# Kernel tuning notes

Hardware: AMD Instinct MI355X
Metric: run time of the kernel (lower is better)

## Reference

```python
import jax, jax.numpy as jnp
import numpy as np
import math

D = 1024
H = 16
EPS = 1e-5

def _layernorm(x, gamma, beta):
    mu = jnp.mean(x, axis=-1, keepdims=True)
    var = jnp.var(x, axis=-1, keepdims=True)
    return (x - mu) * jax.lax.rsqrt(var + EPS) * gamma + beta

def setup_inputs() -> dict:
    key = jax.random.key(0)
    ks = jax.random.split(key, 6)
    B, T = 2, 2048
    x = jax.random.normal(ks[0], (B, T, D), dtype=jnp.float32)
    s = 1.0 / math.sqrt(D)
    Wq = jax.random.normal(ks[1], (D, D), dtype=jnp.float32) * s
    Wk = jax.random.normal(ks[2], (D, D), dtype=jnp.float32) * s
    Wv = jax.random.normal(ks[3], (D, D), dtype=jnp.float32) * s
    gamma = jnp.ones((D,), dtype=jnp.float32)
    beta = jnp.zeros((D,), dtype=jnp.float32)
    return {"x": x, "Wq": Wq, "Wk": Wk, "Wv": Wv, "gamma": gamma, "beta": beta}

def reference(x, Wq, Wk, Wv, gamma, beta):
    B, T, Dm = x.shape
    hd = Dm // H
    xn = _layernorm(x, gamma, beta)
    # torch Linear (no bias): y = x @ W.T
    q = (xn @ Wq.T).reshape(B, T, H, hd)
    k = (xn @ Wk.T).reshape(B, T, H, hd)
    v = (xn @ Wv.T).reshape(B, T, H, hd)
    scale = 1.0 / math.sqrt(hd)
    att = jnp.einsum('bnhd,bmhd->bnmh', q, k) * scale  # B,T,T,H
    w = jax.nn.softmax(att, axis=2)  # softmax over key dim m
    y = jnp.einsum('bnmh,bmhd->bnhd', w, v).reshape(B, T, Dm)
    return x + y
```

## Files before the change

### kernel.cpp

```cpp
#include <hip/hip_runtime.h>
#include <hip/hip_bf16.h>
#include <stdint.h>

#define D_MODEL 1024
#define T_SEQ   2048
#define NB      2
#define NH      16
#define HD      64
#define MTOK    4096

typedef __bf16  bf16x8 __attribute__((ext_vector_type(8)));
typedef float   f32x4  __attribute__((ext_vector_type(4)));
typedef float   f32x16 __attribute__((ext_vector_type(16)));

#define GPTR(p) ((const __attribute__((address_space(1))) void*)(p))
#define LPTR(p) ((__attribute__((address_space(3))) void*)(p))

static __device__ __forceinline__ ushort f2bf(float f) {
    union { float f; uint32_t u; } c{f};
    uint32_t u = c.u;
    return (ushort)((u + 0x7fff + ((u >> 16) & 1)) >> 16);
}

static __device__ __forceinline__ unsigned cvt_pk_bf16(float lo, float hi) {
    unsigned r;
    asm("v_cvt_pk_bf16_f32 %0, %1, %2" : "=v"(r) : "v"(lo), "v"(hi));
    return r;
}

#if defined(__has_builtin)
#if __has_builtin(__builtin_amdgcn_exp2f)
#define FEXP2(x) __builtin_amdgcn_exp2f(x)
#endif
#endif
#ifndef FEXP2
static __device__ __forceinline__ float fexp2_asm(float x) {
    float r;
    asm("v_exp_f32 %0, %1" : "=v"(r) : "v"(x));
    return r;
}
#define FEXP2(x) fexp2_asm(x)
#endif

__global__ __launch_bounds__(256) void ln_kernel(const float* __restrict__ x,
                                                 const float* __restrict__ gamma,
                                                 const float* __restrict__ beta,
                                                 ushort* __restrict__ xn) {
    int row = blockIdx.x;
    int tid = threadIdx.x;
    const float4* xr = (const float4*)(x + (size_t)row * D_MODEL);
    float4 v = xr[tid];
    float s  = v.x + v.y + v.z + v.w;
    float ss = v.x * v.x + v.y * v.y + v.z * v.z + v.w * v.w;
    #pragma unroll
    for (int m = 1; m < 64; m <<= 1) {
        s  += __shfl_xor(s, m);
        ss += __shfl_xor(ss, m);
    }
    __shared__ float red[8];
    int w = tid >> 6, lane = tid & 63;
    if (lane == 0) { red[w] = s; red[4 + w] = ss; }
    __syncthreads();
    s  = red[0] + red[1] + red[2] + red[3];
    ss = red[4] + red[5] + red[6] + red[7];
    float mu   = s * (1.0f / D_MODEL);
    float var  = ss * (1.0f / D_MODEL) - mu * mu;
    float rstd = rsqrtf(var + 1e-5f);
    float4 g = ((const float4*)gamma)[tid];
    float4 b = ((const float4*)beta)[tid];
    ushort4 o;
    o.x = f2bf((v.x - mu) * rstd * g.x + b.x);
    o.y = f2bf((v.y - mu) * rstd * g.y + b.y);
    o.z = f2bf((v.z - mu) * rstd * g.z + b.z);
    o.w = f2bf((v.w - mu) * rstd * g.w + b.w);
    ((ushort4*)(xn + (size_t)row * D_MODEL))[tid] = o;
}

__global__ __launch_bounds__(256) void cvt3_kernel(const float* __restrict__ a0,
                                                   const float* __restrict__ a1,
                                                   const float* __restrict__ a2,
                                                   ushort* __restrict__ o0,
                                                   ushort* __restrict__ o1,
                                                   ushort* __restrict__ o2) {
    int z = blockIdx.y;
    const float* a = (z == 0) ? a0 : (z == 1) ? a1 : a2;
    ushort* o = (z == 0) ? o0 : (z == 1) ? o1 : o2;
    int i = blockIdx.x * 256 + threadIdx.x;
    float4 v = ((const float4*)a)[i];
    ushort4 r;
    r.x = f2bf(v.x); r.y = f2bf(v.y); r.z = f2bf(v.z); r.w = f2bf(v.w);
    ((ushort4*)o)[i] = r;
}

__global__ __launch_bounds__(256) void gemm_qkv(const ushort* __restrict__ A,
                                                const ushort* __restrict__ w0,
                                                const ushort* __restrict__ w1,
                                                const ushort* __restrict__ w2,
                                                ushort* __restrict__ c0,
                                                ushort* __restrict__ c1,
                                                ushort* __restrict__ c2,
                                                int M, int N, int K) {
    const ushort* Bw = (blockIdx.z == 0) ? w0 : (blockIdx.z == 1) ? w1 : w2;
    ushort* C = (blockIdx.z == 0) ? c0 : (blockIdx.z == 1) ? c1 : c2;

    __shared__ __align__(16) ushort lA[128 * 64];
    __shared__ __align__(16) ushort lB[128 * 64];
    int tid = threadIdx.x;
    int w = tid >> 6, lane = tid & 63;
    int wr = w >> 1, wc = w & 1;
    int l15 = lane & 15, l4 = lane >> 4;
    int row0 = blockIdx.x * 128, col0 = blockIdx.y * 128;

    f32x4 zero = {0.f, 0.f, 0.f, 0.f};
    f32x4 acc[4][4];
    #pragma unroll
    for (int i = 0; i < 4; ++i)
        #pragma unroll
        for (int j = 0; j < 4; ++j) acc[i][j] = zero;

    int s_row = (tid * 16) >> 7;
    int s_col = ((tid * 16) & 127) >> 1;

    for (int kt = 0; kt < K / 64; ++kt) {
        int k0 = kt * 64;
        __syncthreads();
        #pragma unroll
        for (int i = 0; i < 4; ++i) {
            int r = s_row + i * 32;
            const ushort* ga = A + (size_t)(row0 + r) * K + k0 + s_col;
            __builtin_amdgcn_global_load_lds(GPTR(ga), LPTR((char*)lA + i * 4096 + w * 1024), 16, 0, 0);
            const ushort* gb = Bw + (size_t)(col0 + r) * K + k0 + s_col;
            __builtin_amdgcn_global_load_lds(GPTR(gb), LPTR((char*)lB + i * 4096 + w * 1024), 16, 0, 0);
        }
        __syncthreads();
        #pragma unroll
        for (int ks = 0; ks < 2; ++ks) {
            bf16x8 af[4], bfr[4];
            #pragma unroll
            for (int i = 0; i < 4; ++i) {
                af[i]  = *(const bf16x8*)&lA[(wr * 64 + i * 16 + l15) * 64 + ks * 32 + l4 * 8];
                bfr[i] = *(const bf16x8*)&lB[(wc * 64 + i * 16 + l15) * 64 + ks * 32 + l4 * 8];
            }
            #pragma unroll
            for (int i = 0; i < 4; ++i)
                #pragma unroll
                for (int j = 0; j < 4; ++j)
                    acc[i][j] = __builtin_amdgcn_mfma_f32_16x16x32_bf16(af[i], bfr[j], acc[i][j], 0, 0, 0);
        }
    }
    if (blockIdx.z == 2) {
        #pragma unroll
        for (int i = 0; i < 4; ++i) {
            int rbase = row0 + wr * 64 + i * 16 + l4 * 4;
            #pragma unroll
            for (int j = 0; j < 4; ++j) {
                int col = col0 + wc * 64 + j * 16 + l15;
                ushort4 o4;
                o4.x = f2bf(acc[i][j][0]);
                o4.y = f2bf(acc[i][j][1]);
                o4.z = f2bf(acc[i][j][2]);
                o4.w = f2bf(acc[i][j][3]);
                *(ushort4*)&C[(size_t)col * M + rbase] = o4;
            }
        }
    } else {
        float sc = (blockIdx.z == 0) ? 0.18033688011112042f : 1.0f;
        #pragma unroll
        for (int i = 0; i < 4; ++i) {
            int rbase = row0 + wr * 64 + i * 16 + l4 * 4;
            #pragma unroll
            for (int j = 0; j < 4; ++j) {
                int col = col0 + wc * 64 + j * 16 + l15;
                #pragma unroll
                for (int r = 0; r < 4; ++r)
                    C[(size_t)(rbase + r) * N + col] = f2bf(acc[i][j][r] * sc);
            }
        }
    }
}

__global__ __launch_bounds__(256, 2) void attn_kernel(const ushort* __restrict__ Q,
                                                      const ushort* __restrict__ Km,
                                                      const ushort* __restrict__ Vt,
                                                      const float* __restrict__ x,
                                                      float* __restrict__ out) {
    int bid = blockIdx.x;
    int sw  = (bid & 7) * 64 + (bid >> 3);
    int qt = sw & 15, h = (sw >> 4) & 15, b = sw >> 8;

    int tid = threadIdx.x, w = tid >> 6, lane = tid & 63;
    int l31 = lane & 31, hh = lane >> 5, x7 = lane & 7;
    size_t head_off = (size_t)b * T_SEQ * D_MODEL + (size_t)h * HD;
    const ushort* Qh  = Q  + head_off;
    const ushort* Kh  = Km + head_off;
    const ushort* Vth = Vt + (size_t)h * HD * MTOK + (size_t)b * T_SEQ;

    __shared__ __align__(16) ushort lK[4][64 * 64];
    __shared__ __align__(16) ushort lV[4][64 * 64];

    int qrow = qt * 128 + w * 32 + l31;
    bf16x8 qf[4];
    #pragma unroll
    for (int c = 0; c < 4; ++c)
        qf[c] = *(const bf16x8*)&Qh[(size_t)qrow * D_MODEL + hh * 8 + c * 16];

    int i0  = w * 128 + lane;
    int r0  = i0 >> 3;
    int cg0 = (i0 & 7) ^ (r0 & 7);
    const ushort* ksrc0 = Kh  + (size_t)r0 * D_MODEL + cg0 * 8;
    const ushort* ksrc1 = ksrc0 + (size_t)8 * D_MODEL;
    const ushort* vsrc0 = Vth + (size_t)r0 * MTOK + cg0 * 8;
    const ushort* vsrc1 = vsrc0 + (size_t)8 * MTOK;

    int chv[4];
    #pragma unroll
    for (int c = 0; c < 4; ++c) chv[c] = ((hh + 2 * c) ^ x7) << 4;

    f32x16 oa[2], ob[2], zvec;
    float la = 0.f, lb = 0.f;
    #pragma unroll
    for (int i = 0; i < 16; ++i) {
        oa[0][i] = 0.f; oa[1][i] = 0.f; ob[0][i] = 0.f; ob[1][i] = 0.f;
        zvec[i] = 0.f;
    }

    auto STAGE = [&](int t) {
        size_t kb = (size_t)t * 64;
        char* dk = (char*)lK[t & 3] + w * 2048;
        char* dv = (char*)lV[t & 3] + w * 2048;
        __builtin_amdgcn_global_load_lds(GPTR(ksrc0 + kb * D_MODEL), LPTR(dk), 16, 0, 0);
        __builtin_amdgcn_global_load_lds(GPTR(ksrc1 + kb * D_MODEL), LPTR(dk + 1024), 16, 0, 0);
        __builtin_amdgcn_global_load_lds(GPTR(vsrc0 + kb), LPTR(dv), 16, 0, 0);
        __builtin_amdgcn_global_load_lds(GPTR(vsrc1 + kb), LPTR(dv + 1024), 16, 0, 0);
    };

    auto QK = [&](int t, f32x16& sa, f32x16& sb) {
        const char* lKc = (const char*)lK[t & 3];
        __builtin_amdgcn_s_setprio(1);
        {
            bf16x8 ka  = *(const bf16x8*)(lKc + l31 * 128 + chv[0]);
            bf16x8 kb2 = *(const bf16x8*)(lKc + (32 + l31) * 128 + chv[0]);
            sa = __builtin_amdgcn_mfma_f32_32x32x16_bf16(ka,  qf[0], zvec, 0, 0, 0);
            sb = __builtin_amdgcn_mfma_f32_32x32x16_bf16(kb2, qf[0], zvec, 0, 0, 0);
        }
        #pragma unroll
        for (int c = 1; c < 4; ++c) {
            bf16x8 ka  = *(const bf16x8*)(lKc + l31 * 128 + chv[c]);
            bf16x8 kb2 = *(const bf16x8*)(lKc + (32 + l31) * 128 + chv[c]);
            sa = __builtin_amdgcn_mfma_f32_32x32x16_bf16(ka,  qf[c], sa, 0, 0, 0);
            sb = __builtin_amdgcn_mfma_f32_32x32x16_bf16(kb2, qf[c], sb, 0, 0, 0);
        }
        __builtin_amdgcn_s_setprio(0);
    };

    auto SMPV = [&](int t, const f32x16& sa, const f32x16& sb) {
        const char* lVc = (const char*)lV[t & 3];
        bf16x8 pfr[4];
        #pragma unroll
        for (int kbb = 0; kbb < 2; ++kbb) {
            float pr[16];
            #pragma unroll
            for (int r = 0; r < 16; ++r) pr[r] = FEXP2(kbb ? sb[r] : sa[r]);
            float s0 = (pr[0] + pr[1]) + (pr[2] + pr[3]);
            float s1 = (pr[4] + pr[5]) + (pr[6] + pr[7]);
            float s2 = (pr[8] + pr[9]) + (pr[10] + pr[11]);
            float s3 = (pr[12] + pr[13]) + (pr[14] + pr[15]);
            if (kbb == 0) la += (s0 + s1) + (s2 + s3);
            else          lb += (s0 + s1) + (s2 + s3);
            #pragma unroll
            for (int sl = 0; sl < 2; ++sl) {
                unsigned pA = cvt_pk_bf16(pr[sl * 8 + 0], pr[sl * 8 + 1]);
                unsigned pB = cvt_pk_bf16(pr[sl * 8 + 2], pr[sl * 8 + 3]);
                unsigned pC = cvt_pk_bf16(pr[sl * 8 + 4], pr[sl * 8 + 5]);
                unsigned pD = cvt_pk_bf16(pr[sl * 8 + 6], pr[sl * 8 + 7]);
                asm("v_permlane32_swap_b32 %0, %1" : "+v"(pA), "+v"(pC));
                asm("v_permlane32_swap_b32 %0, %1" : "+v"(pB), "+v"(pD));
                union { unsigned u[4]; bf16x8 v; } pf;
                pf.u[0] = pA; pf.u[1] = pB; pf.u[2] = pC; pf.u[3] = pD;
                pfr[kbb * 2 + sl] = pf.v;
            }
        }
        __builtin_amdgcn_s_setprio(1);
        #pragma unroll
        for (int ks = 0; ks < 4; ++ks) {
            #pragma unroll
            for (int dblk = 0; dblk < 2; ++dblk) {
                bf16x8 vf = *(const bf16x8*)(lVc + (dblk * 32 + l31) * 128 + chv[ks]);
                if (ks & 1)
                    ob[dblk] = __builtin_amdgcn_mfma_f32_32x32x16_bf16(vf, pfr[ks], ob[dblk], 0, 0, 0);
                else
                    oa[dblk] = __builtin_amdgcn_mfma_f32_32x32x16_bf16(vf, pfr[ks], oa[dblk], 0, 0, 0);
            }
        }
        __builtin_amdgcn_s_setprio(0);
    };

    STAGE(0);
    STAGE(1);
    __syncthreads();

    const int NT = T_SEQ / 64;
    for (int s = 0; s < NT / 2; ++s) {
        int t0 = 2 * s;
        if (s < NT / 2 - 1) { STAGE(t0 + 2); STAGE(t0 + 3); }
        f32x16 sa0, sb0, sa1, sb1;
        QK(t0, sa0, sb0);
        QK(t0 + 1, sa1, sb1);
        SMPV(t0, sa0, sb0);
        SMPV(t0 + 1, sa1, sb1);
        __syncthreads();
    }

    float Lt = la + lb;
    float Lfull = Lt + __shfl_xor(Lt, 32);
    float inv = 1.0f / Lfull;
    const float* xrow = x   + (size_t)(b * T_SEQ + qrow) * D_MODEL + h * HD + 4 * hh;
    float*       orow = out + (size_t)(b * T_SEQ + qrow) * D_MODEL + h * HD + 4 * hh;
    #pragma unroll
    for (int dblk = 0; dblk < 2; ++dblk) {
        #pragma unroll
        for (int g = 0; g < 4; ++g) {
            int coff = dblk * 32 + 8 * g;
            float4 xv = *(const float4*)(xrow + coff);
            float4 ov;
            ov.x = xv.x + (oa[dblk][4 * g + 0] + ob[dblk][4 * g + 0]) * inv;
            ov.y = xv.y + (oa[dblk][4 * g + 1] + ob[dblk][4 * g + 1]) * inv;
            ov.z = xv.z + (oa[dblk][4 * g + 2] + ob[dblk][4 * g + 2]) * inv;
            ov.w = xv.w + (oa[dblk][4 * g + 3] + ob[dblk][4 * g + 3]) * inv;
            *(float4*)(orow + coff) = ov;
        }
    }
}

extern "C" void kernel_launch(void* const* d_in, const int* in_sizes, int n_in,
                              void* d_out, int out_size, void* d_ws, size_t ws_size,
                              hipStream_t stream) {
    const float* x     = (const float*)d_in[0];
    const float* Wq    = (const float*)d_in[1];
    const float* Wk    = (const float*)d_in[2];
    const float* Wv    = (const float*)d_in[3];
    const float* gamma = (const float*)d_in[4];
    const float* beta  = (const float*)d_in[5];
    float* out = (float*)d_out;

    char* ws = (char*)d_ws;
    ushort* xn  = (ushort*)(ws);
    ushort* wqb = (ushort*)(ws + (8  << 20));
    ushort* wkb = (ushort*)(ws + (10 << 20));
    ushort* wvb = (ushort*)(ws + (12 << 20));
    ushort* Qb  = (ushort*)(ws + (14 << 20));
    ushort* Kb  = (ushort*)(ws + (22 << 20));
    ushort* Vtb = (ushort*)(ws + (30 << 20));

    int M = NB * T_SEQ;

    cvt3_kernel<<<dim3(1024, 3), 256, 0, stream>>>(Wq, Wk, Wv, wqb, wkb, wvb);
    ln_kernel<<<dim3(M), 256, 0, stream>>>(x, gamma, beta, xn);
    gemm_qkv<<<dim3(M / 128, D_MODEL / 128, 3), 256, 0, stream>>>(
        xn, wqb, wkb, wvb, Qb, Kb, Vtb, M, D_MODEL, D_MODEL);
    attn_kernel<<<dim3(512), 256, 0, stream>>>(Qb, Kb, Vtb, x, out);
}
```

Baseline: 110.0 us.

## Double-buffer QKV GEMM LDS tiles with XOR swizzle and MFMA priority

The QKV projection GEMM now stages its tiles through double-buffered LDS, prefetching the next K tile while the current one is consumed. This removes one barrier per iteration and overlaps global-to-LDS loads with MFMA work. The LDS layout is XOR-swizzled by row to avoid bank conflicts on fragment reads, and s_setprio raises wave priority around the MFMA section. LDS use doubles to 64KB per block, which may reduce occupancy.

```diff
diff --git a/kernel.cpp b/kernel.cpp
--- a/kernel.cpp
+++ b/kernel.cpp
@@ -103,8 +103,8 @@
     const ushort* Bw = (blockIdx.z == 0) ? w0 : (blockIdx.z == 1) ? w1 : w2;
     ushort* C = (blockIdx.z == 0) ? c0 : (blockIdx.z == 1) ? c1 : c2;
 
-    __shared__ __align__(16) ushort lA[128 * 64];
-    __shared__ __align__(16) ushort lB[128 * 64];
+    __shared__ __align__(16) ushort lA[2][128 * 64];
+    __shared__ __align__(16) ushort lB[2][128 * 64];
     int tid = threadIdx.x;
     int w = tid >> 6, lane = tid & 63;
     int wr = w >> 1, wc = w & 1;
@@ -118,28 +118,43 @@
         #pragma unroll
         for (int j = 0; j < 4; ++j) acc[i][j] = zero;
 
-    int s_row = (tid * 16) >> 7;
-    int s_col = ((tid * 16) & 127) >> 1;
-
-    for (int kt = 0; kt < K / 64; ++kt) {
+    int sr  = tid >> 3;
+    int scc = (((tid & 7) ^ (sr & 7)) << 3);
+    int rch[2];
+    rch[0] = ((l4)     ^ (l15 & 7)) << 4;
+    rch[1] = ((4 + l4) ^ (l15 & 7)) << 4;
+
+    auto STAGE = [&](int buf, int kt) {
         int k0 = kt * 64;
-        __syncthreads();
         #pragma unroll
         for (int i = 0; i < 4; ++i) {
-            int r = s_row + i * 32;
-            const ushort* ga = A + (size_t)(row0 + r) * K + k0 + s_col;
-            __builtin_amdgcn_global_load_lds(GPTR(ga), LPTR((char*)lA + i * 4096 + w * 1024), 16, 0, 0);
-            const ushort* gb = Bw + (size_t)(col0 + r) * K + k0 + s_col;
-            __builtin_amdgcn_global_load_lds(GPTR(gb), LPTR((char*)lB + i * 4096 + w * 1024), 16, 0, 0);
-        }
-        __syncthreads();
+            int r = i * 32 + sr;
+            const ushort* ga = A + (size_t)(row0 + r) * K + k0 + scc;
+            __builtin_amdgcn_global_load_lds(GPTR(ga), LPTR((char*)lA[buf] + i * 4096 + tid * 16), 16, 0, 0);
+            const ushort* gb = Bw + (size_t)(col0 + r) * K + k0 + scc;
+            __builtin_amdgcn_global_load_lds(GPTR(gb), LPTR((char*)lB[buf] + i * 4096 + tid * 16), 16, 0, 0);
+        }
+    };
+
+    STAGE(0, 0);
+    __syncthreads();
+
+    int buf = 0;
+    const int NK = K / 64;
+    for (int kt = 0; kt < NK; ++kt) {
+        if (kt + 1 < NK) STAGE(buf ^ 1, kt + 1);
+        const char* la  = (const char*)lA[buf];
+        const char* lb_ = (const char*)lB[buf];
+        __builtin_amdgcn_s_setprio(1);
         #pragma unroll
         for (int ks = 0; ks < 2; ++ks) {
             bf16x8 af[4], bfr[4];
             #pragma unroll
             for (int i = 0; i < 4; ++i) {
-                af[i]  = *(const bf16x8*)&lA[(wr * 64 + i * 16 + l15) * 64 + ks * 32 + l4 * 8];
-                bfr[i] = *(const bf16x8*)&lB[(wc * 64 + i * 16 + l15) * 64 + ks * 32 + l4 * 8];
+                int ra = wr * 64 + i * 16 + l15;
+                int rb = wc * 64 + i * 16 + l15;
+                af[i]  = *(const bf16x8*)(la  + ra * 128 + rch[ks]);
+                bfr[i] = *(const bf16x8*)(lb_ + rb * 128 + rch[ks]);
             }
             #pragma unroll
             for (int i = 0; i < 4; ++i)
@@ -147,7 +162,11 @@
                 for (int j = 0; j < 4; ++j)
                     acc[i][j] = __builtin_amdgcn_mfma_f32_16x16x32_bf16(af[i], bfr[j], acc[i][j], 0, 0, 0);
         }
-    }
+        __builtin_amdgcn_s_setprio(0);
+        __syncthreads();
+        buf ^= 1;
+    }
+
     if (blockIdx.z == 2) {
         #pragma unroll
         for (int i = 0; i < 4; ++i) {
```

Measured after the change: 99.86 us. -9.2%, faster.
